# Optimization experiments

Hardware: AMD Instinct MI355X
Metric: run time of the kernel (lower is better)

## Reference

```python
import jax, jax.numpy as jnp
import numpy as np

B, S, P, L, H = 64, 512, 32, 30, 768
FH = 1024  # fc_hidden_size


def setup_inputs() -> dict:
    key = jax.random.key(0)
    ks = jax.random.split(key, 8)
    token_embeddings = jax.random.normal(ks[0], (B, S, H), jnp.float32)
    pooler_output = jax.random.normal(ks[1], (B, H), jnp.float32)
    num_positions = jax.random.randint(ks[2], (B, P), 0, S)
    # labels: 0/1 codes, with trailing slots per example padded with -1 rows
    lab = jax.random.randint(ks[3], (B, P, L), 0, 2).astype(jnp.float32)
    valid = jax.random.randint(ks[4], (B, 1), 8, P + 1)  # num real slots per example
    row = jnp.arange(P)[None, :]
    lab = jnp.where((row < valid)[:, :, None], lab, -1.0)
    num_codes_labels = lab.reshape(B, P * L)
    W1 = jax.random.normal(ks[5], (2 * H, FH), jnp.float32) / np.sqrt(2 * H)
    b1 = jnp.zeros((FH,), jnp.float32)
    W2 = jax.random.normal(ks[6], (FH, FH // 2), jnp.float32) / np.sqrt(FH)
    b2 = jnp.zeros((FH // 2,), jnp.float32)
    W3 = jax.random.normal(ks[7], (FH // 2, L), jnp.float32) / np.sqrt(FH // 2)
    b3 = jnp.zeros((L,), jnp.float32)
    return {"token_embeddings": token_embeddings, "pooler_output": pooler_output,
            "num_positions": num_positions, "num_codes_labels": num_codes_labels,
            "W1": W1, "b1": b1, "W2": W2, "b2": b2, "W3": W3, "b3": b3}


def reference(token_embeddings, pooler_output, num_positions, num_codes_labels,
              W1, b1, W2, b2, W3, b3):
    # gather number-token hidden states: [B, P, H]
    p_hidden = jnp.take_along_axis(token_embeddings, num_positions[:, :, None], axis=1)
    feat = jnp.concatenate(
        [p_hidden, jnp.broadcast_to(pooler_output[:, None, :], p_hidden.shape)], axis=-1)
    # Batch_Net_CLS head. NOTE: original uses nn.LeakyReLU(True) -> negative_slope=1.0,
    # which is mathematically the identity, so the activations are omitted (faithful).
    h = feat @ W1 + b1
    h = h @ W2 + b2
    logits = h @ W3 + b3  # [B, P, L]

    labels = num_codes_labels.reshape(B, -1, L)
    pad_pre = jnp.any(labels != -1.0, axis=-1)  # [B, P] True for real slots
    mf = pad_pre.astype(jnp.float32)

    # BCEWithLogitsLoss over non-pad elements: softplus(x) - x*y, mean
    bce_elem = jax.nn.softplus(logits) - logits * labels
    bce_loss = jnp.sum(bce_elem * mf[:, :, None]) / (jnp.sum(mf) * L)

    binary = (jax.nn.sigmoid(logits) > 0.5).astype(jnp.float32)
    count_out = jnp.sum(binary, axis=-1)
    count_lab = jnp.sum(labels, axis=-1)
    count_loss = jnp.mean((count_out - count_lab) ** 2 * mf)

    # position loss: only slots where both counts are exactly 1 (single-hot)
    eq = (count_out == 1.0) & (count_lab == 1.0)
    pos_out = jnp.argmax(binary, axis=-1).astype(jnp.float32)
    pos_lab = jnp.argmax(labels, axis=-1).astype(jnp.float32)
    n_eq = jnp.sum(eq.astype(jnp.float32))
    pos_sum = jnp.sum((pos_out - pos_lab) ** 2 * eq.astype(jnp.float32))
    position_loss = jnp.where(n_eq > 0, pos_sum / jnp.maximum(n_eq, 1.0), 0.0)

    return bce_loss + 10.0 * count_loss + 5.0 * position_loss
```

## Files before the change

### kernel.cpp

```cpp
#include <hip/hip_runtime.h>
#include <cstddef>
#include <cstdint>

#define Mq   2048
#define Lq   30
#define N1q  1024
#define N2q  512
#define K1q  1536
#define Hq   768
#define NBLK 512

typedef float    f32x4 __attribute__((ext_vector_type(4)));
typedef _Float16 f16x8 __attribute__((ext_vector_type(8)));

#define GLD16(gptr, lptr) \
  __builtin_amdgcn_global_load_lds((const __attribute__((address_space(1))) void*)(gptr), \
                                   (__attribute__((address_space(3))) void*)(lptr), 16, 0, 0)

__global__ __launch_bounds__(256)
void prep_a1(const float* __restrict__ tok, const float* __restrict__ pool,
             const int* __restrict__ npos, _Float16* __restrict__ A1) {
  const int m = blockIdx.x;
  const int bI = m >> 5, p = m & 31;
  const int pos = npos[bI * 32 + p];
  const float* src1 = tok + ((size_t)bI * 512 + pos) * Hq;
  const float* src2 = pool + (size_t)bI * Hq;
  _Float16* dst = A1 + (size_t)m * K1q;
  for (int g = threadIdx.x; g < 384; g += 256) {
    const float* s = (g < 192) ? (src1 + g * 4) : (src2 + (g - 192) * 4);
    float4 v = *(const float4*)s;
    __align__(8) _Float16 o[4] = {(_Float16)v.x, (_Float16)v.y, (_Float16)v.z, (_Float16)v.w};
    *(uint2*)(dst + g * 4) = *(const uint2*)o;
  }
}

template<int K, int N>
__global__ __launch_bounds__(256)
void transpose_cvt(const float* __restrict__ src, _Float16* __restrict__ dst) {
  __shared__ float T[64][65];
  const int t = threadIdx.x;
  const int n0 = blockIdx.x * 64, k0 = blockIdx.y * 64;
  {
    const int kl = t >> 2, nc = (t & 3) * 16;
    const float* s = src + (size_t)(k0 + kl) * N + n0 + nc;
    float4 v0 = *(const float4*)s;
    float4 v1 = *(const float4*)(s + 4);
    float4 v2 = *(const float4*)(s + 8);
    float4 v3 = *(const float4*)(s + 12);
    T[nc + 0][kl] = v0.x; T[nc + 1][kl] = v0.y; T[nc + 2][kl] = v0.z; T[nc + 3][kl] = v0.w;
    T[nc + 4][kl] = v1.x; T[nc + 5][kl] = v1.y; T[nc + 6][kl] = v1.z; T[nc + 7][kl] = v1.w;
    T[nc + 8][kl] = v2.x; T[nc + 9][kl] = v2.y; T[nc +10][kl] = v2.z; T[nc +11][kl] = v2.w;
    T[nc +12][kl] = v3.x; T[nc +13][kl] = v3.y; T[nc +14][kl] = v3.z; T[nc +15][kl] = v3.w;
  }
  __syncthreads();
  {
    const int nl = t >> 2, kc = (t & 3) * 16;
    __align__(16) _Float16 tmp[16];
    #pragma unroll
    for (int i = 0; i < 16; ++i) tmp[i] = (_Float16)T[nl][kc + i];
    _Float16* d = dst + (size_t)(n0 + nl) * K + k0 + kc;
    *(uint4*)d       = *(const uint4*)tmp;
    *(uint4*)(d + 8) = *(const uint4*)(tmp + 8);
  }
}

template<int KFULL, int KSLICE, int NC>
__global__ __launch_bounds__(256)
void gemm_f16(const _Float16* __restrict__ A, const _Float16* __restrict__ BT,
              float* __restrict__ Cpart) {
  __shared__ _Float16 As[128 * 32];
  __shared__ _Float16 Bs[128 * 32];
  const int tid = threadIdx.x, w = tid >> 6, lane = tid & 63;
  const int n0 = blockIdx.x * 128, m0 = blockIdx.y * 128, z = blockIdx.z;
  const int ml = lane & 15, g4 = lane >> 4;
  const int wm = (w >> 1) * 64, wn = (w & 1) * 64;

  f32x4 acc[4][4];
  #pragma unroll
  for (int i = 0; i < 4; ++i)
    #pragma unroll
    for (int j = 0; j < 4; ++j)
      #pragma unroll
      for (int r = 0; r < 4; ++r) acc[i][j][r] = 0.f;

  const int rs0 = w * 32 + (lane >> 2);
  const int cl  = lane & 3;

  for (int it = 0; it < KSLICE / 32; ++it) {
    const int kt = z * KSLICE + it * 32;
    __syncthreads();
    #pragma unroll
    for (int t = 0; t < 2; ++t) {
      const int r  = rs0 + t * 16;
      const int cs = cl ^ ((r >> 1) & 3);
      GLD16(A  + (size_t)(m0 + r) * KFULL + kt + cs * 8, As + (w * 32 + t * 16) * 32);
      GLD16(BT + (size_t)(n0 + r) * KFULL + kt + cs * 8, Bs + (w * 32 + t * 16) * 32);
    }
    __syncthreads();
    f16x8 af[4], bf[4];
    #pragma unroll
    for (int i = 0; i < 4; ++i) {
      const int ar = wm + i * 16 + ml;
      af[i] = *(const f16x8*)(As + ar * 32 + ((g4 ^ ((ar >> 1) & 3)) << 3));
      const int br = wn + i * 16 + ml;
      bf[i] = *(const f16x8*)(Bs + br * 32 + ((g4 ^ ((br >> 1) & 3)) << 3));
    }
    #pragma unroll
    for (int i = 0; i < 4; ++i)
      #pragma unroll
      for (int j = 0; j < 4; ++j)
        acc[i][j] = __builtin_amdgcn_mfma_f32_16x16x32_f16(af[i], bf[j], acc[i][j], 0, 0, 0);
  }

  float* Cp = Cpart + (size_t)z * Mq * NC;
  #pragma unroll
  for (int i = 0; i < 4; ++i) {
    const int row0 = m0 + wm + i * 16 + g4 * 4;
    #pragma unroll
    for (int j = 0; j < 4; ++j) {
      const int col = n0 + wn + j * 16 + ml;
      #pragma unroll
      for (int r = 0; r < 4; ++r)
        Cp[(size_t)(row0 + r) * NC + col] = acc[i][j][r];
    }
  }
}

__global__ __launch_bounds__(256)
void combine1(const float* __restrict__ P, const float* __restrict__ b1,
              _Float16* __restrict__ h1) {
  const int idx = (blockIdx.x * 256 + threadIdx.x) * 4;
  const int col = idx & (N1q - 1);
  const size_t MN = (size_t)Mq * N1q;
  float4 v = *(const float4*)(P + idx);
  float4 u = *(const float4*)(P + MN + idx);
  float4 b = *(const float4*)(b1 + col);
  __align__(8) _Float16 o[4] = {
      (_Float16)(v.x + u.x + b.x), (_Float16)(v.y + u.y + b.y),
      (_Float16)(v.z + u.z + b.z), (_Float16)(v.w + u.w + b.w)};
  *(uint2*)(h1 + idx) = *(const uint2*)o;
}

__global__ __launch_bounds__(256)
void loss_kernel(const float* __restrict__ C2, const float* __restrict__ b2,
                 const float* __restrict__ W3, const float* __restrict__ b3,
                 const float* __restrict__ labels, float* __restrict__ part) {
  __shared__ float hrow[4][512];
  __shared__ float red[4][5];
  const int tid = threadIdx.x, w = tid >> 6, lane = tid & 63;
  const int m = blockIdx.x * 4 + w;
  const size_t MN2 = (size_t)Mq * N2q;

  {
    const int k = lane * 8;
    float4 s0 = *(const float4*)(b2 + k);
    float4 s1 = *(const float4*)(b2 + k + 4);
    const float* cp = C2 + (size_t)m * N2q + k;
    #pragma unroll
    for (int z = 0; z < 4; ++z) {
      float4 v0 = *(const float4*)(cp + (size_t)z * MN2);
      float4 v1 = *(const float4*)(cp + (size_t)z * MN2 + 4);
      s0.x += v0.x; s0.y += v0.y; s0.z += v0.z; s0.w += v0.w;
      s1.x += v1.x; s1.y += v1.y; s1.z += v1.z; s1.w += v1.w;
    }
    *(float4*)&hrow[w][k]     = s0;
    *(float4*)&hrow[w][k + 4] = s1;
  }
  __syncthreads();

  const int c  = lane & 31;
  const int kh = lane >> 5;
  float a0 = 0.f, a1 = 0.f, a2 = 0.f, a3 = 0.f;
  if (c < Lq) {
    const float* hp = hrow[w] + kh * 256;
    const float* wp = W3 + (size_t)(kh * 256) * Lq + c;
    #pragma unroll 4
    for (int i = 0; i < 256; i += 4) {
      a0 = fmaf(hp[i],     wp[(i)     * Lq], a0);
      a1 = fmaf(hp[i + 1], wp[(i + 1) * Lq], a1);
      a2 = fmaf(hp[i + 2], wp[(i + 2) * Lq], a2);
      a3 = fmaf(hp[i + 3], wp[(i + 3) * Lq], a3);
    }
  }
  float a = (a0 + a1) + (a2 + a3);
  a += __shfl_xor(a, 32);

  const bool act = lane < Lq;
  float logit = 0.f, lab = 0.f;
  if (act) {
    logit = a + b3[lane];
    lab = labels[(size_t)m * Lq + lane];
  }

  const unsigned long long validmask = __ballot(act && lab != -1.0f);
  const unsigned long long outmask   = __ballot(act && logit > 0.0f);
  const unsigned long long labmask   = __ballot(act && lab == 1.0f);
  const bool valid = (validmask != 0ULL);
  const int count_out = __popcll(outmask);
  const int count_lab = __popcll(labmask);

  float bce = 0.f;
  if (act && valid) {
    const float x = logit;
    bce = fmaxf(x, 0.f) + log1pf(expf(-fabsf(x))) - x * lab;
  }
  bce += __shfl_xor(bce, 16); bce += __shfl_xor(bce, 8);
  bce += __shfl_xor(bce, 4);  bce += __shfl_xor(bce, 2);
  bce += __shfl_xor(bce, 1);

  if (lane == 0) {
    float pb = 0.f, pv = 0.f, pc = 0.f, pe = 0.f, pp = 0.f;
    if (valid) {
      pb = bce; pv = 1.f;
      const float d = (float)count_out - (float)count_lab;
      pc = d * d;
    }
    if (count_out == 1 && count_lab == 1) {
      const float po = (float)(__ffsll((long long)outmask) - 1);
      const float pl = (float)(__ffsll((long long)labmask) - 1);
      pe = 1.f;
      const float dp = po - pl;
      pp = dp * dp;
    }
    red[w][0] = pb; red[w][1] = pv; red[w][2] = pc; red[w][3] = pe; red[w][4] = pp;
  }
  __syncthreads();
  if (tid < 5) {
    part[blockIdx.x * 5 + tid] =
        red[0][tid] + red[1][tid] + red[2][tid] + red[3][tid];
  }
}

__global__ __launch_bounds__(256)
void finalize_kernel(const float* __restrict__ part, float* __restrict__ out) {
  __shared__ float red[32][5];
  const int t = threadIdx.x;
  if (t < 160) {
    const int j = t % 5, grp = t / 5;
    float s = 0.f;
    for (int i = grp; i < NBLK; i += 32) s += part[i * 5 + j];
    red[grp][j] = s;
  }
  __syncthreads();
  if (t < 5) {
    float s = 0.f;
    #pragma unroll
    for (int g = 0; g < 32; ++g) s += red[g][t];
    red[0][t] = s;
  }
  __syncthreads();
  if (t == 0) {
    const float bce = red[0][0] / (red[0][1] * (float)Lq);
    const float cnt = 10.0f * red[0][2] / (float)Mq;
    const float pos = (red[0][3] > 0.f) ? 5.0f * red[0][4] / fmaxf(red[0][3], 1.0f) : 0.f;
    out[0] = bce + cnt + pos;
  }
}

extern "C" void kernel_launch(void* const* d_in, const int* in_sizes, int n_in,
                              void* d_out, int out_size, void* d_ws, size_t ws_size,
                              hipStream_t stream) {
  const float* tok    = (const float*)d_in[0];
  const float* pool   = (const float*)d_in[1];
  const int*   npos   = (const int*)  d_in[2];
  const float* labels = (const float*)d_in[3];
  const float* W1     = (const float*)d_in[4];
  const float* b1     = (const float*)d_in[5];
  const float* W2     = (const float*)d_in[6];
  const float* b2     = (const float*)d_in[7];
  const float* W3     = (const float*)d_in[8];
  const float* b3     = (const float*)d_in[9];
  float* out = (float*)d_out;

  char* ws = (char*)d_ws;
  _Float16* A1   = (_Float16*)(ws + 0x00000000);
  float*    C2p  = (float*)   (ws + 0x00000000);
  float*    C1p  = (float*)   (ws + 0x00600000);
  _Float16* W1T  = (_Float16*)(ws + 0x01600000);
  _Float16* W2T  = (_Float16*)(ws + 0x01A00000);
  _Float16* h1   = (_Float16*)(ws + 0x01B00000);
  float*    part = (float*)   (ws + 0x01F00000);

  prep_a1<<<2048, 256, 0, stream>>>(tok, pool, npos, A1);
  transpose_cvt<K1q, N1q><<<dim3(N1q / 64, K1q / 64), 256, 0, stream>>>(W1, W1T);
  transpose_cvt<N1q, N2q><<<dim3(N2q / 64, N1q / 64), 256, 0, stream>>>(W2, W2T);
  gemm_f16<K1q, 768, N1q><<<dim3(8, 16, 2), 256, 0, stream>>>(A1, W1T, C1p);
  combine1<<<2048, 256, 0, stream>>>(C1p, b1, h1);
  gemm_f16<N1q, 256, N2q><<<dim3(4, 16, 4), 256, 0, stream>>>(h1, W2T, C2p);
  loss_kernel<<<NBLK, 256, 0, stream>>>(C2p, b2, W3, b3, labels, part);
  finalize_kernel<<<1, 256, 0, stream>>>(part, out);
}
```

Before: 204.4 us.

## Merge prep kernels, fuse finalize into loss, raise split-K, vectorize GEMM stores

After: 234.7 us. 14.8% more time.

```diff
diff --git a/kernel.cpp b/kernel.cpp
--- a/kernel.cpp
+++ b/kernel.cpp
@@ -9,6 +9,8 @@
 #define K1q  1536
 #define Hq   768
 #define NBLK 512
+#define Z1   4
+#define Z2   8
 
 typedef float    f32x4 __attribute__((ext_vector_type(4)));
 typedef _Float16 f16x8 __attribute__((ext_vector_type(8)));
@@ -17,29 +19,11 @@
   __builtin_amdgcn_global_load_lds((const __attribute__((address_space(1))) void*)(gptr), \
                                    (__attribute__((address_space(3))) void*)(lptr), 16, 0, 0)
 
-__global__ __launch_bounds__(256)
-void prep_a1(const float* __restrict__ tok, const float* __restrict__ pool,
-             const int* __restrict__ npos, _Float16* __restrict__ A1) {
-  const int m = blockIdx.x;
-  const int bI = m >> 5, p = m & 31;
-  const int pos = npos[bI * 32 + p];
-  const float* src1 = tok + ((size_t)bI * 512 + pos) * Hq;
-  const float* src2 = pool + (size_t)bI * Hq;
-  _Float16* dst = A1 + (size_t)m * K1q;
-  for (int g = threadIdx.x; g < 384; g += 256) {
-    const float* s = (g < 192) ? (src1 + g * 4) : (src2 + (g - 192) * 4);
-    float4 v = *(const float4*)s;
-    __align__(8) _Float16 o[4] = {(_Float16)v.x, (_Float16)v.y, (_Float16)v.z, (_Float16)v.w};
-    *(uint2*)(dst + g * 4) = *(const uint2*)o;
-  }
-}
-
-template<int K, int N>
-__global__ __launch_bounds__(256)
-void transpose_cvt(const float* __restrict__ src, _Float16* __restrict__ dst) {
+__device__ void transpose_tile(const float* __restrict__ src,
+                               _Float16* __restrict__ dst,
+                               int K, int N, int k0, int n0) {
   __shared__ float T[64][65];
   const int t = threadIdx.x;
-  const int n0 = blockIdx.x * 64, k0 = blockIdx.y * 64;
   {
     const int kl = t >> 2, nc = (t & 3) * 16;
     const float* s = src + (size_t)(k0 + kl) * N + n0 + nc;
@@ -64,6 +48,37 @@
   }
 }
 
+__global__ __launch_bounds__(256)
+void prep_all(const float* __restrict__ tok, const float* __restrict__ pool,
+              const int* __restrict__ npos, const float* __restrict__ W1,
+              const float* __restrict__ W2, _Float16* __restrict__ A1,
+              _Float16* __restrict__ W1T, _Float16* __restrict__ W2T,
+              int* __restrict__ counter) {
+  const int bid = blockIdx.x, tid = threadIdx.x;
+  if (bid == 0 && tid == 0) *counter = 0;
+  if (bid < 256) {
+    const int q = tid >> 5, l32 = tid & 31;
+    const int m = bid * 8 + q;
+    const int bI = m >> 5, p = m & 31;
+    const int pos = npos[bI * 32 + p];
+    const float* src1 = tok + ((size_t)bI * 512 + pos) * Hq;
+    const float* src2 = pool + (size_t)bI * Hq;
+    _Float16* dst = A1 + (size_t)m * K1q;
+    for (int g = l32; g < 384; g += 32) {
+      const float* s = (g < 192) ? (src1 + g * 4) : (src2 + (g - 192) * 4);
+      float4 v = *(const float4*)s;
+      __align__(8) _Float16 o[4] = {(_Float16)v.x, (_Float16)v.y, (_Float16)v.z, (_Float16)v.w};
+      *(uint2*)(dst + g * 4) = *(const uint2*)o;
+    }
+  } else if (bid < 640) {
+    const int idx = bid - 256;
+    transpose_tile(W1, W1T, K1q, N1q, (idx / 16) * 64, (idx % 16) * 64);
+  } else {
+    const int idx = bid - 640;
+    transpose_tile(W2, W2T, N1q, N2q, (idx / 8) * 64, (idx % 8) * 64);
+  }
+}
+
 template<int KFULL, int KSLICE, int NC>
 __global__ __launch_bounds__(256)
 void gemm_f16(const _Float16* __restrict__ A, const _Float16* __restrict__ BT,
@@ -109,19 +124,17 @@
     for (int i = 0; i < 4; ++i)
       #pragma unroll
       for (int j = 0; j < 4; ++j)
-        acc[i][j] = __builtin_amdgcn_mfma_f32_16x16x32_f16(af[i], bf[j], acc[i][j], 0, 0, 0);
+        acc[i][j] = __builtin_amdgcn_mfma_f32_16x16x32_f16(bf[j], af[i], acc[i][j], 0, 0, 0);
   }
 
   float* Cp = Cpart + (size_t)z * Mq * NC;
   #pragma unroll
   for (int i = 0; i < 4; ++i) {
-    const int row0 = m0 + wm + i * 16 + g4 * 4;
+    const int row = m0 + wm + i * 16 + ml;
     #pragma unroll
     for (int j = 0; j < 4; ++j) {
-      const int col = n0 + wn + j * 16 + ml;
-      #pragma unroll
-      for (int r = 0; r < 4; ++r)
-        Cp[(size_t)(row0 + r) * NC + col] = acc[i][j][r];
+      const int col = n0 + wn + j * 16 + g4 * 4;
+      *(float4*)(Cp + (size_t)row * NC + col) = *(const float4*)&acc[i][j];
     }
   }
 }
@@ -132,21 +145,25 @@
   const int idx = (blockIdx.x * 256 + threadIdx.x) * 4;
   const int col = idx & (N1q - 1);
   const size_t MN = (size_t)Mq * N1q;
-  float4 v = *(const float4*)(P + idx);
-  float4 u = *(const float4*)(P + MN + idx);
-  float4 b = *(const float4*)(b1 + col);
-  __align__(8) _Float16 o[4] = {
-      (_Float16)(v.x + u.x + b.x), (_Float16)(v.y + u.y + b.y),
-      (_Float16)(v.z + u.z + b.z), (_Float16)(v.w + u.w + b.w)};
+  float4 s = *(const float4*)(b1 + col);
+  #pragma unroll
+  for (int z = 0; z < Z1; ++z) {
+    float4 v = *(const float4*)(P + (size_t)z * MN + idx);
+    s.x += v.x; s.y += v.y; s.z += v.z; s.w += v.w;
+  }
+  __align__(8) _Float16 o[4] = {(_Float16)s.x, (_Float16)s.y, (_Float16)s.z, (_Float16)s.w};
   *(uint2*)(h1 + idx) = *(const uint2*)o;
 }
 
 __global__ __launch_bounds__(256)
 void loss_kernel(const float* __restrict__ C2, const float* __restrict__ b2,
                  const float* __restrict__ W3, const float* __restrict__ b3,
-                 const float* __restrict__ labels, float* __restrict__ part) {
+                 const float* __restrict__ labels, float* __restrict__ part,
+                 int* __restrict__ counter, float* __restrict__ out) {
   __shared__ float hrow[4][512];
   __shared__ float red[4][5];
+  __shared__ float fred[32][5];
+  __shared__ int lastFlag;
   const int tid = threadIdx.x, w = tid >> 6, lane = tid & 63;
   const int m = blockIdx.x * 4 + w;
   const size_t MN2 = (size_t)Mq * N2q;
@@ -157,7 +174,7 @@
     float4 s1 = *(const float4*)(b2 + k + 4);
     const float* cp = C2 + (size_t)m * N2q + k;
     #pragma unroll
-    for (int z = 0; z < 4; ++z) {
+    for (int z = 0; z < Z2; ++z) {
       float4 v0 = *(const float4*)(cp + (size_t)z * MN2);
       float4 v1 = *(const float4*)(cp + (size_t)z * MN2 + 4);
       s0.x += v0.x; s0.y += v0.y; s0.z += v0.z; s0.w += v0.w;
@@ -229,31 +246,32 @@
     part[blockIdx.x * 5 + tid] =
         red[0][tid] + red[1][tid] + red[2][tid] + red[3][tid];
   }
-}
-
-__global__ __launch_bounds__(256)
-void finalize_kernel(const float* __restrict__ part, float* __restrict__ out) {
-  __shared__ float red[32][5];
-  const int t = threadIdx.x;
-  if (t < 160) {
-    const int j = t % 5, grp = t / 5;
-    float s = 0.f;
-    for (int i = grp; i < NBLK; i += 32) s += part[i * 5 + j];
-    red[grp][j] = s;
+  __threadfence();
+  if (tid == 0) {
+    const int old = atomicAdd(counter, 1);
+    lastFlag = (old == (int)gridDim.x - 1);
   }
   __syncthreads();
-  if (t < 5) {
-    float s = 0.f;
-    #pragma unroll
-    for (int g = 0; g < 32; ++g) s += red[g][t];
-    red[0][t] = s;
-  }
-  __syncthreads();
-  if (t == 0) {
-    const float bce = red[0][0] / (red[0][1] * (float)Lq);
-    const float cnt = 10.0f * red[0][2] / (float)Mq;
-    const float pos = (red[0][3] > 0.f) ? 5.0f * red[0][4] / fmaxf(red[0][3], 1.0f) : 0.f;
-    out[0] = bce + cnt + pos;
+  if (lastFlag) {
+    if (tid < 160) {
+      const int j = tid % 5, grp = tid / 5;
+      float s = 0.f;
+      for (int i = grp; i < NBLK; i += 32) s += part[i * 5 + j];
+      fred[grp][j] = s;
+    }
+    __syncthreads();
+    if (tid == 0) {
+      float t0 = 0.f, t1 = 0.f, t2 = 0.f, t3 = 0.f, t4 = 0.f;
+      #pragma unroll
+      for (int g = 0; g < 32; ++g) {
+        t0 += fred[g][0]; t1 += fred[g][1]; t2 += fred[g][2];
+        t3 += fred[g][3]; t4 += fred[g][4];
+      }
+      const float bceL = t0 / (t1 * (float)Lq);
+      const float cntL = 10.0f * t2 / (float)Mq;
+      const float posL = (t3 > 0.f) ? 5.0f * t4 / fmaxf(t3, 1.0f) : 0.f;
+      out[0] = bceL + cntL + posL;
+    }
   }
 }
 
@@ -276,17 +294,15 @@
   _Float16* A1   = (_Float16*)(ws + 0x00000000);
   float*    C2p  = (float*)   (ws + 0x00000000);
   float*    C1p  = (float*)   (ws + 0x00600000);
-  _Float16* W1T  = (_Float16*)(ws + 0x01600000);
-  _Float16* W2T  = (_Float16*)(ws + 0x01A00000);
-  _Float16* h1   = (_Float16*)(ws + 0x01B00000);
-  float*    part = (float*)   (ws + 0x01F00000);
-
-  prep_a1<<<2048, 256, 0, stream>>>(tok, pool, npos, A1);
-  transpose_cvt<K1q, N1q><<<dim3(N1q / 64, K1q / 64), 256, 0, stream>>>(W1, W1T);
-  transpose_cvt<N1q, N2q><<<dim3(N2q / 64, N1q / 64), 256, 0, stream>>>(W2, W2T);
-  gemm_f16<K1q, 768, N1q><<<dim3(8, 16, 2), 256, 0, stream>>>(A1, W1T, C1p);
+  _Float16* W1T  = (_Float16*)(ws + 0x02600000);
+  _Float16* W2T  = (_Float16*)(ws + 0x02A00000);
+  _Float16* h1   = (_Float16*)(ws + 0x02E00000);
+  float*    part = (float*)   (ws + 0x03200000);
+  int*      cnt  = (int*)     (ws + 0x03210000);
+
+  prep_all<<<768, 256, 0, stream>>>(tok, pool, npos, W1, W2, A1, W1T, W2T, cnt);
+  gemm_f16<K1q, K1q / Z1, N1q><<<dim3(8, 16, Z1), 256, 0, stream>>>(A1, W1T, C1p);
   combine1<<<2048, 256, 0, stream>>>(C1p, b1, h1);
-  gemm_f16<N1q, 256, N2q><<<dim3(4, 16, 4), 256, 0, stream>>>(h1, W2T, C2p);
-  loss_kernel<<<NBLK, 256, 0, stream>>>(C2p, b2, W3, b3, labels, part);
-  finalize_kernel<<<1, 256, 0, stream>>>(part, out);
-}
+  gemm_f16<N1q, N1q / Z2, N2q><<<dim3(4, 16, Z2), 256, 0, stream>>>(h1, W2T, C2p);
+  loss_kernel<<<NBLK, 256, 0, stream>>>(C2p, b2, W3, b3, labels, part, cnt, out);
+}
```
